# Kernel optimization log

Measured on AMD Instinct MI355X. Metric: run time of the kernel, lower is better.

## Reference

```python
import jax, jax.numpy as jnp
import numpy as np

WINDOW = 128  # window_size from init_kwargs
D = 1024      # input_dim
S = 8192      # seq_len


def setup_inputs() -> dict:
    key = jax.random.key(0)
    k1, k2, k3, k4, k5 = jax.random.split(key, 5)
    bound = 1.0 / np.sqrt(D)
    x = jax.random.normal(k1, (1, S, D), dtype=jnp.float32)
    Wq = jax.random.uniform(k2, (D, D), minval=-bound, maxval=bound, dtype=jnp.float32)
    bq = jax.random.uniform(k3, (D,), minval=-bound, maxval=bound, dtype=jnp.float32)
    Wk = jax.random.uniform(k4, (D, D), minval=-bound, maxval=bound, dtype=jnp.float32)
    bk = jax.random.uniform(k5, (D,), minval=-bound, maxval=bound, dtype=jnp.float32)
    return {"x": x, "Wq": Wq, "bq": bq, "Wk": Wk, "bk": bk}


def reference(x, Wq, bq, Wk, bk):
    # x: [1, S, D]  (original code only works with batch==1)
    xs = x[0]                          # [S, D]
    q = xs @ Wq.T + bq                 # [S, D]
    k = xs @ Wk.T + bk                 # [S, D]
    scores = q @ k.T                   # [S, S] dense, matches original buffer
    t = jnp.arange(S)[:, None]
    s = jnp.arange(S)[None, :]
    # original writes scores only for s in [t-WINDOW, t+WINDOW); elsewhere stays 0
    inwin = (s >= t - WINDOW) & (s < t + WINDOW)
    scores = jnp.where(inwin, scores, 0.0)
    attn = jax.nn.softmax(scores, axis=1)  # softmax INCLUDES the zero entries, as in original
    out = attn @ xs                    # [S, D]
    return out
```

## Files before the change

kernel.cpp:

```cpp
#include <hip/hip_runtime.h>

#define S 8192
#define D 1024
#define WINDOW 128
#define TQ 16
#define UMAX 288
#define BK 32
#define PAD 68
#define BAND 384

typedef __attribute__((ext_vector_type(8))) short short8;
typedef __attribute__((ext_vector_type(4))) float floatx4;
typedef __attribute__((ext_vector_type(4))) unsigned short ushort4v;
typedef unsigned short u16t;

__device__ __forceinline__ float wave_sum(float v) {
  #pragma unroll
  for (int off = 32; off > 0; off >>= 1) v += __shfl_xor(v, off, 64);
  return v;
}
__device__ __forceinline__ float wave_max(float v) {
  #pragma unroll
  for (int off = 32; off > 0; off >>= 1) v = fmaxf(v, __shfl_xor(v, off, 64));
  return v;
}
__device__ __forceinline__ unsigned int f2bf_rn(float f) {
  unsigned int u = __float_as_uint(f);
  return (u + 0x7fffu + ((u >> 16) & 1u)) >> 16;
}

__global__ __launch_bounds__(256) void split_kernel(
    const float* __restrict__ src, u16t* __restrict__ hi, u16t* __restrict__ lo)
{
  int i = (blockIdx.x * 256 + threadIdx.x) * 4;
  float4 v = *(const float4*)(src + i);
  float f[4] = {v.x, v.y, v.z, v.w};
  ushort4v h, l;
  #pragma unroll
  for (int c = 0; c < 4; ++c) {
    unsigned int hb = f2bf_rn(f[c]);
    float hf = __uint_as_float(hb << 16);
    unsigned int lb = f2bf_rn(f[c] - hf);
    h[c] = (u16t)hb;
    l[c] = (u16t)lb;
  }
  *(ushort4v*)(hi + i) = h;
  *(ushort4v*)(lo + i) = l;
}

__global__ __launch_bounds__(256) void transpose_x(const float* __restrict__ x,
                                                   u16t* __restrict__ xT)
{
  __shared__ float tile[64][65];
  const int s0 = blockIdx.x * 64;
  const int d0 = blockIdx.y * 64;
  const int t = threadIdx.x;
  #pragma unroll
  for (int p = 0; p < 4; ++p) {
    int r = (t >> 4) + p * 16;
    int c = (t & 15) * 4;
    float4 v = *(const float4*)(x + (size_t)(s0 + r) * D + d0 + c);
    tile[r][c+0] = v.x; tile[r][c+1] = v.y; tile[r][c+2] = v.z; tile[r][c+3] = v.w;
  }
  __syncthreads();
  #pragma unroll
  for (int p = 0; p < 4; ++p) {
    int dd = (t >> 4) + p * 16;
    int ss = (t & 15) * 4;
    ushort4v o;
    #pragma unroll
    for (int u = 0; u < 4; ++u) o[u] = (u16t)f2bf_rn(tile[ss + u][dd]);
    *(ushort4v*)(xT + (size_t)(d0 + dd) * S + s0 + ss) = o;
  }
}

__global__ __launch_bounds__(256) void gemm_qk(
    const u16t* __restrict__ xhi, const u16t* __restrict__ xlo,
    const u16t* __restrict__ wqhi, const u16t* __restrict__ wqlo,
    const u16t* __restrict__ wkhi, const u16t* __restrict__ wklo,
    const float* __restrict__ bqv, const float* __restrict__ bkv,
    u16t* __restrict__ qh, u16t* __restrict__ ql,
    u16t* __restrict__ kh, u16t* __restrict__ kl)
{
  __shared__ __align__(16) u16t Ah[128 * BK];
  __shared__ __align__(16) u16t Al[128 * BK];
  __shared__ __align__(16) u16t Bh[128 * BK];
  __shared__ __align__(16) u16t Bl[128 * BK];

  const int tid  = threadIdx.x;
  const int lane = tid & 63;
  const int wv   = tid >> 6;
  const int t0   = blockIdx.x * 128;
  const int n0   = blockIdx.y * 128;

  const u16t* whi = blockIdx.z ? wkhi : wqhi;
  const u16t* wlo = blockIdx.z ? wklo : wqlo;
  const float* bias = blockIdx.z ? bkv : bqv;
  u16t* oh = blockIdx.z ? kh : qh;
  u16t* ol = blockIdx.z ? kl : ql;

  floatx4 acc[4][4] = {};

  const int m0w  = (wv & 1) * 64;
  const int n0w  = (wv >> 1) * 64;
  const int srow = lane >> 2;
  const int scol = (((lane & 3) ^ ((lane >> 3) & 3))) * 8;
  const int p8   = (((lane >> 4) ^ ((lane >> 1) & 3))) * 8;

  for (int k0 = 0; k0 < D; k0 += BK) {
    __syncthreads();
    #pragma unroll
    for (int sg = 0; sg < 2; ++sg) {
      int seg  = wv * 2 + sg;
      int arow = t0 + seg * 16 + srow;
      int brow = n0 + seg * 16 + srow;
      size_t ga = (size_t)arow * D + k0 + scol;
      size_t gb = (size_t)brow * D + k0 + scol;
      __builtin_amdgcn_global_load_lds(
          (const __attribute__((address_space(1))) void*)(xhi + ga),
          (__attribute__((address_space(3))) void*)(&Ah[seg * 512]), 16, 0, 0);
      __builtin_amdgcn_global_load_lds(
          (const __attribute__((address_space(1))) void*)(xlo + ga),
          (__attribute__((address_space(3))) void*)(&Al[seg * 512]), 16, 0, 0);
      __builtin_amdgcn_global_load_lds(
          (const __attribute__((address_space(1))) void*)(whi + gb),
          (__attribute__((address_space(3))) void*)(&Bh[seg * 512]), 16, 0, 0);
      __builtin_amdgcn_global_load_lds(
          (const __attribute__((address_space(1))) void*)(wlo + gb),
          (__attribute__((address_space(3))) void*)(&Bl[seg * 512]), 16, 0, 0);
    }
    __syncthreads();

    short8 ah[4], al[4], bh[4], bl[4];
    #pragma unroll
    for (int t = 0; t < 4; ++t) {
      int ar = (m0w + t * 16 + (lane & 15)) * BK + p8;
      int br = (n0w + t * 16 + (lane & 15)) * BK + p8;
      ah[t] = *(const short8*)&Ah[ar];
      al[t] = *(const short8*)&Al[ar];
      bh[t] = *(const short8*)&Bh[br];
      bl[t] = *(const short8*)&Bl[br];
    }
    #pragma unroll
    for (int mt = 0; mt < 4; ++mt)
      #pragma unroll
      for (int nt = 0; nt < 4; ++nt) {
        acc[mt][nt] = __builtin_amdgcn_mfma_f32_16x16x32_bf16(ah[mt], bh[nt], acc[mt][nt], 0, 0, 0);
        acc[mt][nt] = __builtin_amdgcn_mfma_f32_16x16x32_bf16(ah[mt], bl[nt], acc[mt][nt], 0, 0, 0);
        acc[mt][nt] = __builtin_amdgcn_mfma_f32_16x16x32_bf16(al[mt], bh[nt], acc[mt][nt], 0, 0, 0);
      }
  }

  #pragma unroll
  for (int mt = 0; mt < 4; ++mt) {
    #pragma unroll
    for (int nt = 0; nt < 4; ++nt) {
      int n = n0 + n0w + nt * 16 + (lane & 15);
      int m = t0 + m0w + mt * 16 + (lane >> 4) * 4;
      float b = bias[n];
      #pragma unroll
      for (int r = 0; r < 4; ++r) {
        float v = acc[mt][nt][r] + b;
        unsigned int hb = f2bf_rn(v);
        float hf = __uint_as_float(hb << 16);
        unsigned int lb = f2bf_rn(v - hf);
        size_t idx = (size_t)(m + r) * D + n;
        oh[idx] = (u16t)hb;
        ol[idx] = (u16t)lb;
      }
    }
  }
}

__global__ __launch_bounds__(256) void colsum_kernel(const float* __restrict__ x,
                                                     float* __restrict__ xsum)
{
  int d = blockIdx.x * 256 + threadIdx.x;
  int tbase = blockIdx.y * 256;
  float s = 0.f;
  for (int t = 0; t < 256; ++t) s += x[(size_t)(tbase + t) * D + d];
  atomicAdd(&xsum[d], s);
}

__global__ __launch_bounds__(256) void scores_kernel(
    const u16t* __restrict__ qh, const u16t* __restrict__ ql,
    const u16t* __restrict__ kh, const u16t* __restrict__ kl,
    float* __restrict__ band)
{
  __shared__ __align__(16) u16t Ah[128 * BK];
  __shared__ __align__(16) u16t Al[128 * BK];
  __shared__ __align__(16) u16t Bh[128 * BK];
  __shared__ __align__(16) u16t Bl[128 * BK];

  const int tid  = threadIdx.x;
  const int lane = tid & 63;
  const int wv   = tid >> 6;
  const int t0   = blockIdx.x * 128;
  const int jt   = blockIdx.y;
  const int s_base = t0 - 128 + jt * 128;

  floatx4 acc[4][4] = {};

  const int m0w  = (wv & 1) * 64;
  const int n0w  = (wv >> 1) * 64;
  const int srow = lane >> 2;
  const int scol = (((lane & 3) ^ ((lane >> 3) & 3))) * 8;
  const int p8   = (((lane >> 4) ^ ((lane >> 1) & 3))) * 8;

  for (int k0 = 0; k0 < D; k0 += BK) {
    __syncthreads();
    #pragma unroll
    for (int sg = 0; sg < 2; ++sg) {
      int seg  = wv * 2 + sg;
      int arow = t0 + seg * 16 + srow;
      int brow = s_base + seg * 16 + srow;
      brow = min(max(brow, 0), S - 1);
      size_t ga = (size_t)arow * D + k0 + scol;
      size_t gb = (size_t)brow * D + k0 + scol;
      __builtin_amdgcn_global_load_lds(
          (const __attribute__((address_space(1))) void*)(qh + ga),
          (__attribute__((address_space(3))) void*)(&Ah[seg * 512]), 16, 0, 0);
      __builtin_amdgcn_global_load_lds(
          (const __attribute__((address_space(1))) void*)(ql + ga),
          (__attribute__((address_space(3))) void*)(&Al[seg * 512]), 16, 0, 0);
      __builtin_amdgcn_global_load_lds(
          (const __attribute__((address_space(1))) void*)(kh + gb),
          (__attribute__((address_space(3))) void*)(&Bh[seg * 512]), 16, 0, 0);
      __builtin_amdgcn_global_load_lds(
          (const __attribute__((address_space(1))) void*)(kl + gb),
          (__attribute__((address_space(3))) void*)(&Bl[seg * 512]), 16, 0, 0);
    }
    __syncthreads();

    short8 ah[4], al[4], bh[4], bl[4];
    #pragma unroll
    for (int t = 0; t < 4; ++t) {
      int ar = (m0w + t * 16 + (lane & 15)) * BK + p8;
      int br = (n0w + t * 16 + (lane & 15)) * BK + p8;
      ah[t] = *(const short8*)&Ah[ar];
      al[t] = *(const short8*)&Al[ar];
      bh[t] = *(const short8*)&Bh[br];
      bl[t] = *(const short8*)&Bl[br];
    }
    #pragma unroll
    for (int mt = 0; mt < 4; ++mt)
      #pragma unroll
      for (int nt = 0; nt < 4; ++nt) {
        acc[mt][nt] = __builtin_amdgcn_mfma_f32_16x16x32_bf16(ah[mt], bh[nt], acc[mt][nt], 0, 0, 0);
        acc[mt][nt] = __builtin_amdgcn_mfma_f32_16x16x32_bf16(ah[mt], bl[nt], acc[mt][nt], 0, 0, 0);
        acc[mt][nt] = __builtin_amdgcn_mfma_f32_16x16x32_bf16(al[mt], bh[nt], acc[mt][nt], 0, 0, 0);
      }
  }

  #pragma unroll
  for (int mt = 0; mt < 4; ++mt) {
    #pragma unroll
    for (int nt = 0; nt < 4; ++nt) {
      int n_loc = n0w + nt * 16 + (lane & 15);
      int s = s_base + n_loc;
      #pragma unroll
      for (int r = 0; r < 4; ++r) {
        int m_loc = m0w + mt * 16 + (lane >> 4) * 4 + r;
        int t = t0 + m_loc;
        bool inwin = (s >= t - WINDOW) && (s < t + WINDOW) && (s >= 0) && (s < S);
        band[(size_t)t * BAND + jt * 128 + n_loc] = inwin ? acc[mt][nt][r] : 0.f;
      }
    }
  }
}

__global__ __launch_bounds__(256) void softmax_kernel(
    const float* __restrict__ band, u16t* __restrict__ Pb, float* __restrict__ e0d)
{
  const int lane = threadIdx.x & 63;
  const int w    = threadIdx.x >> 6;
  const int t    = blockIdx.x * 4 + w;
  const float* row = band + (size_t)t * BAND;

  float v[6];
  float mx = 0.f;
  #pragma unroll
  for (int i = 0; i < 6; ++i) {
    v[i] = row[i * 64 + lane];
    mx = fmaxf(mx, v[i]);
  }
  mx = wave_max(mx);
  float e0 = __expf(-mx);
  float ss = 0.f;
  #pragma unroll
  for (int i = 0; i < 6; ++i) {
    v[i] = __expf(v[i] - mx);
    ss += v[i];
  }
  ss = wave_sum(ss);
  float dinv = 1.f / (ss + (float)(S - BAND) * e0);
  #pragma unroll
  for (int i = 0; i < 6; ++i)
    Pb[(size_t)t * BAND + i * 64 + lane] = (u16t)f2bf_rn((v[i] - e0) * dinv);
  if (lane == 0) e0d[t] = e0 * dinv;
}

__global__ __launch_bounds__(256) void pv_kernel(
    const u16t* __restrict__ Pb, const u16t* __restrict__ xT,
    const float* __restrict__ e0d, const float* __restrict__ xsum,
    float* __restrict__ out)
{
  __shared__ __align__(16) u16t Ab[128 * BK];
  __shared__ __align__(16) u16t Bb[128 * BK];

  const int tid  = threadIdx.x;
  const int lane = tid & 63;
  const int wv   = tid >> 6;
  const int t0   = blockIdx.x * 128;
  const int d0   = blockIdx.y * 128;
  const int origin = t0 - 128;

  floatx4 acc[4][4] = {};

  const int m0w  = (wv & 1) * 64;
  const int n0w  = (wv >> 1) * 64;
  const int srow = lane >> 2;
  const int scol = (((lane & 3) ^ ((lane >> 3) & 3))) * 8;
  const int p8   = (((lane >> 4) ^ ((lane >> 1) & 3))) * 8;

  for (int k0 = 0; k0 < BAND; k0 += BK) {
    __syncthreads();
    #pragma unroll
    for (int sg = 0; sg < 2; ++sg) {
      int seg  = wv * 2 + sg;
      int arow = t0 + seg * 16 + srow;
      int brow = d0 + seg * 16 + srow;
      int s_g  = origin + k0 + scol;
      s_g = min(max(s_g, 0), S - 8);
      size_t ga = (size_t)arow * BAND + k0 + scol;
      size_t gb = (size_t)brow * S + s_g;
      __builtin_amdgcn_global_load_lds(
          (const __attribute__((address_space(1))) void*)(Pb + ga),
          (__attribute__((address_space(3))) void*)(&Ab[seg * 512]), 16, 0, 0);
      __builtin_amdgcn_global_load_lds(
          (const __attribute__((address_space(1))) void*)(xT + gb),
          (__attribute__((address_space(3))) void*)(&Bb[seg * 512]), 16, 0, 0);
    }
    __syncthreads();

    short8 af[4], bf[4];
    #pragma unroll
    for (int t = 0; t < 4; ++t) {
      int ar = (m0w + t * 16 + (lane & 15)) * BK + p8;
      int br = (n0w + t * 16 + (lane & 15)) * BK + p8;
      af[t] = *(const short8*)&Ab[ar];
      bf[t] = *(const short8*)&Bb[br];
    }
    #pragma unroll
    for (int mt = 0; mt < 4; ++mt)
      #pragma unroll
      for (int nt = 0; nt < 4; ++nt)
        acc[mt][nt] = __builtin_amdgcn_mfma_f32_16x16x32_bf16(af[mt], bf[nt], acc[mt][nt], 0, 0, 0);
  }

  #pragma unroll
  for (int mt = 0; mt < 4; ++mt) {
    #pragma unroll
    for (int nt = 0; nt < 4; ++nt) {
      int n_g = d0 + n0w + nt * 16 + (lane & 15);
      float xs = xsum[n_g];
      #pragma unroll
      for (int r = 0; r < 4; ++r) {
        int m_g = t0 + m0w + mt * 16 + (lane >> 4) * 4 + r;
        out[(size_t)m_g * D + n_g] = acc[mt][nt][r] + e0d[m_g] * xs;
      }
    }
  }
}

__global__ __launch_bounds__(256) void proj_kernel(
    const float* __restrict__ x, const float* __restrict__ Wq,
    const float* __restrict__ bqv, const float* __restrict__ Wk,
    const float* __restrict__ bkv, float* __restrict__ qout,
    float* __restrict__ kout)
{
  __shared__ __align__(16) float xs[BK][PAD];
  __shared__ __align__(16) float wqs[BK][PAD];
  __shared__ __align__(16) float wks[BK][PAD];
  const int tid = threadIdx.x;
  const int tx = tid & 15, ty = tid >> 4;
  const int t0 = blockIdx.x * 64, i0 = blockIdx.y * 64;
  float accq[4][4] = {}, acck[4][4] = {};
  const int lrow0 = tid >> 3, lc4 = (tid & 7) * 4;
  for (int k0 = 0; k0 < D; k0 += BK) {
    __syncthreads();
    #pragma unroll
    for (int p = 0; p < 2; ++p) {
      int row = lrow0 + p * 32;
      float4 a = *(const float4*)(x  + (size_t)(t0 + row) * D + k0 + lc4);
      float4 b = *(const float4*)(Wq + (size_t)(i0 + row) * D + k0 + lc4);
      float4 c = *(const float4*)(Wk + (size_t)(i0 + row) * D + k0 + lc4);
      xs [lc4+0][row]=a.x; xs [lc4+1][row]=a.y; xs [lc4+2][row]=a.z; xs [lc4+3][row]=a.w;
      wqs[lc4+0][row]=b.x; wqs[lc4+1][row]=b.y; wqs[lc4+2][row]=b.z; wqs[lc4+3][row]=b.w;
      wks[lc4+0][row]=c.x; wks[lc4+1][row]=c.y; wks[lc4+2][row]=c.z; wks[lc4+3][row]=c.w;
    }
    __syncthreads();
    #pragma unroll
    for (int kk = 0; kk < BK; ++kk) {
      float4 av = *(const float4*)&xs [kk][ty*4];
      float4 bv = *(const float4*)&wqs[kk][tx*4];
      float4 cv = *(const float4*)&wks[kk][tx*4];
      float a[4] = {av.x, av.y, av.z, av.w};
      float b[4] = {bv.x, bv.y, bv.z, bv.w};
      float c[4] = {cv.x, cv.y, cv.z, cv.w};
      #pragma unroll
      for (int r = 0; r < 4; ++r)
        #pragma unroll
        for (int cc = 0; cc < 4; ++cc) {
          accq[r][cc] = fmaf(a[r], b[cc], accq[r][cc]);
          acck[r][cc] = fmaf(a[r], c[cc], acck[r][cc]);
        }
    }
  }
  float4 bq4 = *(const float4*)(bqv + i0 + tx*4);
  float4 bk4 = *(const float4*)(bkv + i0 + tx*4);
  #pragma unroll
  for (int r = 0; r < 4; ++r) {
    int trow = t0 + ty*4 + r;
    float4 oq = { accq[r][0]+bq4.x, accq[r][1]+bq4.y, accq[r][2]+bq4.z, accq[r][3]+bq4.w };
    float4 ok = { acck[r][0]+bk4.x, acck[r][1]+bk4.y, acck[r][2]+bk4.z, acck[r][3]+bk4.w };
    *(float4*)(qout + (size_t)trow * D + i0 + tx*4) = oq;
    *(float4*)(kout + (size_t)trow * D + i0 + tx*4) = ok;
  }
}

__global__ __launch_bounds__(256) void attn_kernel(
    const float* __restrict__ x, const float* __restrict__ q,
    const float* __restrict__ kmat, const float* __restrict__ xsum,
    float* __restrict__ out)
{
  __shared__ __align__(16) float scl[TQ][UMAX];
  __shared__ float e0s[TQ], dinv[TQ];
  const int tid = threadIdx.x, lane = tid & 63, wv = tid >> 6;
  const int t0 = blockIdx.x * TQ;
  const int lo_u = max(0, t0 - WINDOW);
  const int hi_u = min(S, t0 + TQ - 1 + WINDOW);
  const int ucnt = hi_u - lo_u;
  for (int i = tid; i < TQ * UMAX; i += 256) (&scl[0][0])[i] = 0.f;
  __syncthreads();
  {
    const int tiB = wv * 4;
    float4 qf[4][4];
    #pragma unroll
    for (int g = 0; g < 4; ++g) {
      int t = t0 + tiB + g;
      #pragma unroll
      for (int j = 0; j < 4; ++j)
        qf[g][j] = *(const float4*)(q + (size_t)t * D + lane*4 + j*256);
    }
    const int wlo = max(0, t0 + tiB - WINDOW);
    const int whi = min(S, t0 + tiB + 3 + WINDOW);
    for (int s = wlo; s < whi; ++s) {
      float4 kf[4];
      #pragma unroll
      for (int j = 0; j < 4; ++j)
        kf[j] = *(const float4*)(kmat + (size_t)s * D + lane*4 + j*256);
      float acc[4];
      #pragma unroll
      for (int g = 0; g < 4; ++g) {
        float v = 0.f;
        #pragma unroll
        for (int j = 0; j < 4; ++j) {
          v = fmaf(qf[g][j].x, kf[j].x, v);
          v = fmaf(qf[g][j].y, kf[j].y, v);
          v = fmaf(qf[g][j].z, kf[j].z, v);
          v = fmaf(qf[g][j].w, kf[j].w, v);
        }
        acc[g] = v;
      }
      #pragma unroll
      for (int g = 0; g < 4; ++g) {
        float tot = wave_sum(acc[g]);
        int t = t0 + tiB + g;
        if (lane == 0 && s >= t - WINDOW && s < t + WINDOW)
          scl[tiB + g][s - lo_u] = tot;
      }
    }
  }
  __syncthreads();
  #pragma unroll
  for (int g = 0; g < 4; ++g) {
    int ti = wv * 4 + g;
    int t = t0 + ti;
    int lo = max(0, t - WINDOW), hi = min(S, t + WINDOW);
    int cnt = hi - lo, off = lo - lo_u;
    float m = 0.f;
    for (int i = lane; i < cnt; i += 64) m = fmaxf(m, scl[ti][off + i]);
    m = wave_max(m);
    float e0 = __expf(-m);
    float ssum = 0.f;
    for (int i = lane; i < cnt; i += 64) {
      float e = __expf(scl[ti][off + i] - m);
      ssum += e;
      scl[ti][off + i] = e - e0;
    }
    ssum = wave_sum(ssum);
    if (lane == 0) {
      dinv[ti] = 1.f / (ssum + (float)(S - cnt) * e0);
      e0s[ti] = e0;
    }
  }
  __syncthreads();
  {
    const int c4 = tid * 4;
    float4 acc[TQ];
    #pragma unroll
    for (int ti = 0; ti < TQ; ++ti) acc[ti] = make_float4(0.f, 0.f, 0.f, 0.f);
    for (int su = 0; su < ucnt; su += 4) {
      float4 xr[4];
      #pragma unroll
      for (int u = 0; u < 4; ++u)
        xr[u] = *(const float4*)(x + (size_t)(lo_u + su + u) * D + c4);
      #pragma unroll
      for (int ti = 0; ti < TQ; ++ti) {
        float4 w4 = *(const float4*)&scl[ti][su];
        float wvv[4] = {w4.x, w4.y, w4.z, w4.w};
        #pragma unroll
        for (int u = 0; u < 4; ++u) {
          acc[ti].x = fmaf(wvv[u], xr[u].x, acc[ti].x);
          acc[ti].y = fmaf(wvv[u], xr[u].y, acc[ti].y);
          acc[ti].z = fmaf(wvv[u], xr[u].z, acc[ti].z);
          acc[ti].w = fmaf(wvv[u], xr[u].w, acc[ti].w);
        }
      }
    }
    float4 xsv = *(const float4*)(xsum + c4);
    #pragma unroll
    for (int ti = 0; ti < TQ; ++ti) {
      float e0 = e0s[ti], di = dinv[ti];
      float4 o;
      o.x = (acc[ti].x + e0 * xsv.x) * di;
      o.y = (acc[ti].y + e0 * xsv.y) * di;
      o.z = (acc[ti].z + e0 * xsv.z) * di;
      o.w = (acc[ti].w + e0 * xsv.w) * di;
      *(float4*)(out + (size_t)(t0 + ti) * D + c4) = o;
    }
  }
}

extern "C" void kernel_launch(void* const* d_in, const int* in_sizes, int n_in,
                              void* d_out, int out_size, void* d_ws, size_t ws_size,
                              hipStream_t stream) {
  const float* x  = (const float*)d_in[0];
  const float* Wq = (const float*)d_in[1];
  const float* bq = (const float*)d_in[2];
  const float* Wk = (const float*)d_in[3];
  const float* bk = (const float*)d_in[4];
  float* outp = (float*)d_out;

  const size_t SD = (size_t)S * D;
  const size_t DD = (size_t)D * D;

  float* xsum = (float*)d_ws;
  u16t* xhi = (u16t*)(xsum + D);
  u16t* xlo = xhi + SD;
  u16t* wqh = xlo + SD;
  u16t* wql = wqh + DD;
  u16t* wkh = wql + DD;
  u16t* wkl = wkh + DD;
  u16t* qh  = wkl + DD;
  u16t* ql  = qh + SD;
  u16t* kh  = ql + SD;
  u16t* kl  = kh + SD;
  u16t* xT  = kl + SD;
  size_t needed = (size_t)((char*)(xT + SD) - (char*)d_ws);

  float* band = (float*)xhi;
  u16t*  Pb   = xlo;
  float* e0d  = (float*)(Pb + (size_t)S * BAND);

  hipMemsetAsync(xsum, 0, D * sizeof(float), stream);
  colsum_kernel<<<dim3(D / 256, S / 256), 256, 0, stream>>>(x, xsum);

  if (ws_size >= needed) {
    split_kernel<<<SD / 1024, 256, 0, stream>>>(x,  xhi, xlo);
    split_kernel<<<DD / 1024, 256, 0, stream>>>(Wq, wqh, wql);
    split_kernel<<<DD / 1024, 256, 0, stream>>>(Wk, wkh, wkl);
    transpose_x<<<dim3(S / 64, D / 64), 256, 0, stream>>>(x, xT);
    gemm_qk<<<dim3(S / 128, D / 128, 2), 256, 0, stream>>>(
        xhi, xlo, wqh, wql, wkh, wkl, bq, bk, qh, ql, kh, kl);
    scores_kernel<<<dim3(S / 128, 3), 256, 0, stream>>>(qh, ql, kh, kl, band);
    softmax_kernel<<<S / 4, 256, 0, stream>>>(band, Pb, e0d);
    pv_kernel<<<dim3(S / 128, D / 128), 256, 0, stream>>>(Pb, xT, e0d, xsum, outp);
  } else {
    float* q    = (float*)(xsum + D);
    float* kbuf = q + SD;
    proj_kernel<<<dim3(S / 64, D / 64), 256, 0, stream>>>(x, Wq, bq, Wk, bk, q, kbuf);
    attn_kernel<<<S / TQ, 256, 0, stream>>>(x, q, kbuf, xsum, outp);
  }
}
```

Before: 297.0 us.

## Reassociate scores as x·(WqᵀWk)·xᵀ plus bias terms and fuse prep kernels

Rewrites q·kᵀ as x·M·xᵀ plus rank-one bias terms, with M = Wqᵀ·Wk. This replaces the two S×D×D projection GEMMs with one D×D×D GEMM and a single S×D×D GEMM. The x split, transpose, column sum and the a/b bias dot products are fused into one prep kernel. It also drops the XOR LDS swizzle in all MFMA kernels, which may bring back bank conflicts. Workspace use grows, so a smaller workspace would take the slow fallback path.

```diff
diff --git a/kernel.cpp b/kernel.cpp
--- a/kernel.cpp
+++ b/kernel.cpp
@@ -29,27 +29,32 @@
   return (u + 0x7fffu + ((u >> 16) & 1u)) >> 16;
 }
 
-__global__ __launch_bounds__(256) void split_kernel(
-    const float* __restrict__ src, u16t* __restrict__ hi, u16t* __restrict__ lo)
-{
-  int i = (blockIdx.x * 256 + threadIdx.x) * 4;
-  float4 v = *(const float4*)(src + i);
-  float f[4] = {v.x, v.y, v.z, v.w};
-  ushort4v h, l;
-  #pragma unroll
-  for (int c = 0; c < 4; ++c) {
-    unsigned int hb = f2bf_rn(f[c]);
-    float hf = __uint_as_float(hb << 16);
-    unsigned int lb = f2bf_rn(f[c] - hf);
-    h[c] = (u16t)hb;
-    l[c] = (u16t)lb;
-  }
-  *(ushort4v*)(hi + i) = h;
-  *(ushort4v*)(lo + i) = l;
-}
-
-__global__ __launch_bounds__(256) void transpose_x(const float* __restrict__ x,
-                                                   u16t* __restrict__ xT)
+__global__ __launch_bounds__(256) void uv_kernel(
+    const float* __restrict__ Wq, const float* __restrict__ Wk,
+    const float* __restrict__ bq, const float* __restrict__ bk,
+    float* __restrict__ u, float* __restrict__ v, float* __restrict__ cbuf)
+{
+  const int i = blockIdx.x * 256 + threadIdx.x;
+  const int n0 = blockIdx.y * 128;
+  float us = 0.f, vs = 0.f;
+  for (int n = n0; n < n0 + 128; ++n) {
+    us += Wq[(size_t)n * D + i] * bk[n];
+    vs += Wk[(size_t)n * D + i] * bq[n];
+  }
+  atomicAdd(&u[i], us);
+  atomicAdd(&v[i], vs);
+  if (blockIdx.x == 0 && blockIdx.y == 0) {
+    float cs = 0.f;
+    for (int n = threadIdx.x; n < D; n += 256) cs += bq[n] * bk[n];
+    atomicAdd(cbuf, cs);
+  }
+}
+
+__global__ __launch_bounds__(256) void prep_kernel(
+    const float* __restrict__ x, const float* __restrict__ u,
+    const float* __restrict__ v, u16t* __restrict__ xhi, u16t* __restrict__ xlo,
+    u16t* __restrict__ xT, float* __restrict__ xsum,
+    float* __restrict__ a, float* __restrict__ b)
 {
   __shared__ float tile[64][65];
   const int s0 = blockIdx.x * 64;
@@ -59,8 +64,20 @@
   for (int p = 0; p < 4; ++p) {
     int r = (t >> 4) + p * 16;
     int c = (t & 15) * 4;
-    float4 v = *(const float4*)(x + (size_t)(s0 + r) * D + d0 + c);
-    tile[r][c+0] = v.x; tile[r][c+1] = v.y; tile[r][c+2] = v.z; tile[r][c+3] = v.w;
+    float4 vv = *(const float4*)(x + (size_t)(s0 + r) * D + d0 + c);
+    float f[4] = {vv.x, vv.y, vv.z, vv.w};
+    tile[r][c+0] = vv.x; tile[r][c+1] = vv.y; tile[r][c+2] = vv.z; tile[r][c+3] = vv.w;
+    ushort4v h, l;
+    #pragma unroll
+    for (int e = 0; e < 4; ++e) {
+      unsigned int hb = f2bf_rn(f[e]);
+      float hf = __uint_as_float(hb << 16);
+      h[e] = (u16t)hb;
+      l[e] = (u16t)f2bf_rn(f[e] - hf);
+    }
+    size_t idx = (size_t)(s0 + r) * D + d0 + c;
+    *(ushort4v*)(xhi + idx) = h;
+    *(ushort4v*)(xlo + idx) = l;
   }
   __syncthreads();
   #pragma unroll
@@ -69,18 +86,141 @@
     int ss = (t & 15) * 4;
     ushort4v o;
     #pragma unroll
-    for (int u = 0; u < 4; ++u) o[u] = (u16t)f2bf_rn(tile[ss + u][dd]);
+    for (int e = 0; e < 4; ++e) o[e] = (u16t)f2bf_rn(tile[ss + e][dd]);
     *(ushort4v*)(xT + (size_t)(d0 + dd) * S + s0 + ss) = o;
   }
-}
-
-__global__ __launch_bounds__(256) void gemm_qk(
+  if (t < 64) {
+    float s = 0.f;
+    #pragma unroll 8
+    for (int r = 0; r < 64; ++r) s += tile[r][t];
+    atomicAdd(&xsum[d0 + t], s);
+  } else if (t < 128) {
+    int r = t - 64;
+    float s = 0.f;
+    for (int c = 0; c < 64; ++c) s += tile[r][c] * u[d0 + c];
+    atomicAdd(&a[s0 + r], s);
+  } else if (t < 192) {
+    int r = t - 128;
+    float s = 0.f;
+    for (int c = 0; c < 64; ++c) s += tile[r][c] * v[d0 + c];
+    atomicAdd(&b[s0 + r], s);
+  }
+}
+
+__global__ __launch_bounds__(256) void transposeW_kernel(
+    const float* __restrict__ Wq, const float* __restrict__ Wk,
+    u16t* __restrict__ wqth, u16t* __restrict__ wqtl,
+    u16t* __restrict__ wkth, u16t* __restrict__ wktl)
+{
+  __shared__ float tile[64][65];
+  const float* W = blockIdx.z ? Wk : Wq;
+  u16t* oh = blockIdx.z ? wkth : wqth;
+  u16t* ol = blockIdx.z ? wktl : wqtl;
+  const int n0 = blockIdx.x * 64;
+  const int i0 = blockIdx.y * 64;
+  const int t = threadIdx.x;
+  #pragma unroll
+  for (int p = 0; p < 4; ++p) {
+    int r = (t >> 4) + p * 16;
+    int c = (t & 15) * 4;
+    float4 vv = *(const float4*)(W + (size_t)(n0 + r) * D + i0 + c);
+    tile[r][c+0] = vv.x; tile[r][c+1] = vv.y; tile[r][c+2] = vv.z; tile[r][c+3] = vv.w;
+  }
+  __syncthreads();
+  #pragma unroll
+  for (int p = 0; p < 4; ++p) {
+    int ii = (t >> 4) + p * 16;
+    int nn = (t & 15) * 4;
+    ushort4v h, l;
+    #pragma unroll
+    for (int e = 0; e < 4; ++e) {
+      float f = tile[nn + e][ii];
+      unsigned int hb = f2bf_rn(f);
+      float hf = __uint_as_float(hb << 16);
+      h[e] = (u16t)hb;
+      l[e] = (u16t)f2bf_rn(f - hf);
+    }
+    size_t idx = (size_t)(i0 + ii) * D + n0 + nn;
+    *(ushort4v*)(oh + idx) = h;
+    *(ushort4v*)(ol + idx) = l;
+  }
+}
+
+__global__ __launch_bounds__(256) void m_kernel(
+    const u16t* __restrict__ wqth, const u16t* __restrict__ wqtl,
+    const u16t* __restrict__ wkth, const u16t* __restrict__ wktl,
+    u16t* __restrict__ mh, u16t* __restrict__ ml)
+{
+  __shared__ __align__(16) u16t Mbuf[4][64 * BK];
+
+  const int tid  = threadIdx.x;
+  const int lane = tid & 63;
+  const int wv   = tid >> 6;
+  const int i0   = blockIdx.x * 64;
+  const int j0   = blockIdx.y * 64;
+
+  floatx4 acc[2][2] = {};
+  const int m0w = (wv & 1) * 32;
+  const int n0w = (wv >> 1) * 32;
+  const int srow = lane >> 2;
+  const int scol = (lane & 3) * 8;
+
+  for (int k0 = 0; k0 < D; k0 += BK) {
+    __syncthreads();
+    {
+      const u16t* src = (wv == 0) ? wqth : (wv == 1) ? wqtl : (wv == 2) ? wkth : wktl;
+      const int base  = (wv < 2) ? i0 : j0;
+      #pragma unroll
+      for (int sg = 0; sg < 4; ++sg) {
+        int row = base + sg * 16 + srow;
+        size_t g = (size_t)row * D + k0 + scol;
+        __builtin_amdgcn_global_load_lds(
+            (const __attribute__((address_space(1))) void*)(src + g),
+            (__attribute__((address_space(3))) void*)(&Mbuf[wv][sg * 512]), 16, 0, 0);
+      }
+    }
+    __syncthreads();
+    short8 ah[2], al[2], bh[2], bl[2];
+    #pragma unroll
+    for (int t = 0; t < 2; ++t) {
+      int ar = (m0w + t * 16 + (lane & 15)) * BK + (lane >> 4) * 8;
+      int br = (n0w + t * 16 + (lane & 15)) * BK + (lane >> 4) * 8;
+      ah[t] = *(const short8*)&Mbuf[0][ar];
+      al[t] = *(const short8*)&Mbuf[1][ar];
+      bh[t] = *(const short8*)&Mbuf[2][br];
+      bl[t] = *(const short8*)&Mbuf[3][br];
+    }
+    #pragma unroll
+    for (int mt = 0; mt < 2; ++mt)
+      #pragma unroll
+      for (int nt = 0; nt < 2; ++nt) {
+        acc[mt][nt] = __builtin_amdgcn_mfma_f32_16x16x32_bf16(ah[mt], bh[nt], acc[mt][nt], 0, 0, 0);
+        acc[mt][nt] = __builtin_amdgcn_mfma_f32_16x16x32_bf16(ah[mt], bl[nt], acc[mt][nt], 0, 0, 0);
+        acc[mt][nt] = __builtin_amdgcn_mfma_f32_16x16x32_bf16(al[mt], bh[nt], acc[mt][nt], 0, 0, 0);
+      }
+  }
+  #pragma unroll
+  for (int mt = 0; mt < 2; ++mt)
+    #pragma unroll
+    for (int nt = 0; nt < 2; ++nt) {
+      int j = j0 + n0w + nt * 16 + (lane & 15);
+      int i = i0 + m0w + mt * 16 + (lane >> 4) * 4;
+      #pragma unroll
+      for (int r = 0; r < 4; ++r) {
+        float f = acc[mt][nt][r];
+        unsigned int hb = f2bf_rn(f);
+        float hf = __uint_as_float(hb << 16);
+        size_t idx = (size_t)(i + r) * D + j;
+        mh[idx] = (u16t)hb;
+        ml[idx] = (u16t)f2bf_rn(f - hf);
+      }
+    }
+}
+
+__global__ __launch_bounds__(256) void y_kernel(
     const u16t* __restrict__ xhi, const u16t* __restrict__ xlo,
-    const u16t* __restrict__ wqhi, const u16t* __restrict__ wqlo,
-    const u16t* __restrict__ wkhi, const u16t* __restrict__ wklo,
-    const float* __restrict__ bqv, const float* __restrict__ bkv,
-    u16t* __restrict__ qh, u16t* __restrict__ ql,
-    u16t* __restrict__ kh, u16t* __restrict__ kl)
+    const u16t* __restrict__ mhp, const u16t* __restrict__ mlp,
+    u16t* __restrict__ yh, u16t* __restrict__ yl)
 {
   __shared__ __align__(16) u16t Ah[128 * BK];
   __shared__ __align__(16) u16t Al[128 * BK];
@@ -90,30 +230,22 @@
   const int tid  = threadIdx.x;
   const int lane = tid & 63;
   const int wv   = tid >> 6;
-  const int t0   = blockIdx.x * 128;
-  const int n0   = blockIdx.y * 128;
-
-  const u16t* whi = blockIdx.z ? wkhi : wqhi;
-  const u16t* wlo = blockIdx.z ? wklo : wqlo;
-  const float* bias = blockIdx.z ? bkv : bqv;
-  u16t* oh = blockIdx.z ? kh : qh;
-  u16t* ol = blockIdx.z ? kl : ql;
+  const int s0   = blockIdx.x * 128;
+  const int i0   = blockIdx.y * 128;
 
   floatx4 acc[4][4] = {};
-
   const int m0w  = (wv & 1) * 64;
   const int n0w  = (wv >> 1) * 64;
   const int srow = lane >> 2;
-  const int scol = (((lane & 3) ^ ((lane >> 3) & 3))) * 8;
-  const int p8   = (((lane >> 4) ^ ((lane >> 1) & 3))) * 8;
+  const int scol = (lane & 3) * 8;
 
   for (int k0 = 0; k0 < D; k0 += BK) {
     __syncthreads();
     #pragma unroll
     for (int sg = 0; sg < 2; ++sg) {
       int seg  = wv * 2 + sg;
-      int arow = t0 + seg * 16 + srow;
-      int brow = n0 + seg * 16 + srow;
+      int arow = s0 + seg * 16 + srow;
+      int brow = i0 + seg * 16 + srow;
       size_t ga = (size_t)arow * D + k0 + scol;
       size_t gb = (size_t)brow * D + k0 + scol;
       __builtin_amdgcn_global_load_lds(
@@ -123,19 +255,18 @@
           (const __attribute__((address_space(1))) void*)(xlo + ga),
           (__attribute__((address_space(3))) void*)(&Al[seg * 512]), 16, 0, 0);
       __builtin_amdgcn_global_load_lds(
-          (const __attribute__((address_space(1))) void*)(whi + gb),
+          (const __attribute__((address_space(1))) void*)(mhp + gb),
           (__attribute__((address_space(3))) void*)(&Bh[seg * 512]), 16, 0, 0);
       __builtin_amdgcn_global_load_lds(
-          (const __attribute__((address_space(1))) void*)(wlo + gb),
+          (const __attribute__((address_space(1))) void*)(mlp + gb),
           (__attribute__((address_space(3))) void*)(&Bl[seg * 512]), 16, 0, 0);
     }
     __syncthreads();
-
     short8 ah[4], al[4], bh[4], bl[4];
     #pragma unroll
     for (int t = 0; t < 4; ++t) {
-      int ar = (m0w + t * 16 + (lane & 15)) * BK + p8;
-      int br = (n0w + t * 16 + (lane & 15)) * BK + p8;
+      int ar = (m0w + t * 16 + (lane & 15)) * BK + (lane >> 4) * 8;
+      int br = (n0w + t * 16 + (lane & 15)) * BK + (lane >> 4) * 8;
       ah[t] = *(const short8*)&Ah[ar];
       al[t] = *(const short8*)&Al[ar];
       bh[t] = *(const short8*)&Bh[br];
@@ -150,42 +281,29 @@
         acc[mt][nt] = __builtin_amdgcn_mfma_f32_16x16x32_bf16(al[mt], bh[nt], acc[mt][nt], 0, 0, 0);
       }
   }
-
-  #pragma unroll
-  for (int mt = 0; mt < 4; ++mt) {
+  #pragma unroll
+  for (int mt = 0; mt < 4; ++mt)
     #pragma unroll
     for (int nt = 0; nt < 4; ++nt) {
-      int n = n0 + n0w + nt * 16 + (lane & 15);
-      int m = t0 + m0w + mt * 16 + (lane >> 4) * 4;
-      float b = bias[n];
+      int i = i0 + n0w + nt * 16 + (lane & 15);
+      int s = s0 + m0w + mt * 16 + (lane >> 4) * 4;
       #pragma unroll
       for (int r = 0; r < 4; ++r) {
-        float v = acc[mt][nt][r] + b;
-        unsigned int hb = f2bf_rn(v);
+        float f = acc[mt][nt][r];
+        unsigned int hb = f2bf_rn(f);
         float hf = __uint_as_float(hb << 16);
-        unsigned int lb = f2bf_rn(v - hf);
-        size_t idx = (size_t)(m + r) * D + n;
-        oh[idx] = (u16t)hb;
-        ol[idx] = (u16t)lb;
-      }
-    }
-  }
-}
-
-__global__ __launch_bounds__(256) void colsum_kernel(const float* __restrict__ x,
-                                                     float* __restrict__ xsum)
-{
-  int d = blockIdx.x * 256 + threadIdx.x;
-  int tbase = blockIdx.y * 256;
-  float s = 0.f;
-  for (int t = 0; t < 256; ++t) s += x[(size_t)(tbase + t) * D + d];
-  atomicAdd(&xsum[d], s);
+        size_t idx = (size_t)(s + r) * D + i;
+        yh[idx] = (u16t)hb;
+        yl[idx] = (u16t)f2bf_rn(f - hf);
+      }
+    }
 }
 
 __global__ __launch_bounds__(256) void scores_kernel(
-    const u16t* __restrict__ qh, const u16t* __restrict__ ql,
-    const u16t* __restrict__ kh, const u16t* __restrict__ kl,
-    float* __restrict__ band)
+    const u16t* __restrict__ xhi, const u16t* __restrict__ xlo,
+    const u16t* __restrict__ yh, const u16t* __restrict__ yl,
+    const float* __restrict__ a, const float* __restrict__ b,
+    const float* __restrict__ cbuf, float* __restrict__ band)
 {
   __shared__ __align__(16) u16t Ah[128 * BK];
   __shared__ __align__(16) u16t Al[128 * BK];
@@ -198,14 +316,13 @@
   const int t0   = blockIdx.x * 128;
   const int jt   = blockIdx.y;
   const int s_base = t0 - 128 + jt * 128;
+  const float cval = cbuf[0];
 
   floatx4 acc[4][4] = {};
-
   const int m0w  = (wv & 1) * 64;
   const int n0w  = (wv >> 1) * 64;
   const int srow = lane >> 2;
-  const int scol = (((lane & 3) ^ ((lane >> 3) & 3))) * 8;
-  const int p8   = (((lane >> 4) ^ ((lane >> 1) & 3))) * 8;
+  const int scol = (lane & 3) * 8;
 
   for (int k0 = 0; k0 < D; k0 += BK) {
     __syncthreads();
@@ -218,25 +335,24 @@
       size_t ga = (size_t)arow * D + k0 + scol;
       size_t gb = (size_t)brow * D + k0 + scol;
       __builtin_amdgcn_global_load_lds(
-          (const __attribute__((address_space(1))) void*)(qh + ga),
+          (const __attribute__((address_space(1))) void*)(xhi + ga),
           (__attribute__((address_space(3))) void*)(&Ah[seg * 512]), 16, 0, 0);
       __builtin_amdgcn_global_load_lds(
-          (const __attribute__((address_space(1))) void*)(ql + ga),
+          (const __attribute__((address_space(1))) void*)(xlo + ga),
           (__attribute__((address_space(3))) void*)(&Al[seg * 512]), 16, 0, 0);
       __builtin_amdgcn_global_load_lds(
-          (const __attribute__((address_space(1))) void*)(kh + gb),
+          (const __attribute__((address_space(1))) void*)(yh + gb),
           (__attribute__((address_space(3))) void*)(&Bh[seg * 512]), 16, 0, 0);
       __builtin_amdgcn_global_load_lds(
-          (const __attribute__((address_space(1))) void*)(kl + gb),
+          (const __attribute__((address_space(1))) void*)(yl + gb),
           (__attribute__((address_space(3))) void*)(&Bl[seg * 512]), 16, 0, 0);
     }
     __syncthreads();
-
     short8 ah[4], al[4], bh[4], bl[4];
     #pragma unroll
     for (int t = 0; t < 4; ++t) {
-      int ar = (m0w + t * 16 + (lane & 15)) * BK + p8;
-      int br = (n0w + t * 16 + (lane & 15)) * BK + p8;
+      int ar = (m0w + t * 16 + (lane & 15)) * BK + (lane >> 4) * 8;
+      int br = (n0w + t * 16 + (lane & 15)) * BK + (lane >> 4) * 8;
       ah[t] = *(const short8*)&Ah[ar];
       al[t] = *(const short8*)&Al[ar];
       bh[t] = *(const short8*)&Bh[br];
@@ -251,22 +367,22 @@
         acc[mt][nt] = __builtin_amdgcn_mfma_f32_16x16x32_bf16(al[mt], bh[nt], acc[mt][nt], 0, 0, 0);
       }
   }
-
-  #pragma unroll
-  for (int mt = 0; mt < 4; ++mt) {
+  #pragma unroll
+  for (int mt = 0; mt < 4; ++mt)
     #pragma unroll
     for (int nt = 0; nt < 4; ++nt) {
       int n_loc = n0w + nt * 16 + (lane & 15);
       int s = s_base + n_loc;
+      float bv = (s >= 0 && s < S) ? b[s] : 0.f;
       #pragma unroll
       for (int r = 0; r < 4; ++r) {
         int m_loc = m0w + mt * 16 + (lane >> 4) * 4 + r;
         int t = t0 + m_loc;
         bool inwin = (s >= t - WINDOW) && (s < t + WINDOW) && (s >= 0) && (s < S);
-        band[(size_t)t * BAND + jt * 128 + n_loc] = inwin ? acc[mt][nt][r] : 0.f;
-      }
-    }
-  }
+        float sv = inwin ? (acc[mt][nt][r] + a[t] + bv + cval) : 0.f;
+        band[(size_t)t * BAND + jt * 128 + n_loc] = sv;
+      }
+    }
 }
 
 __global__ __launch_bounds__(256) void softmax_kernel(
@@ -276,7 +392,6 @@
   const int w    = threadIdx.x >> 6;
   const int t    = blockIdx.x * 4 + w;
   const float* row = band + (size_t)t * BAND;
-
   float v[6];
   float mx = 0.f;
   #pragma unroll
@@ -316,12 +431,10 @@
   const int origin = t0 - 128;
 
   floatx4 acc[4][4] = {};
-
   const int m0w  = (wv & 1) * 64;
   const int n0w  = (wv >> 1) * 64;
   const int srow = lane >> 2;
-  const int scol = (((lane & 3) ^ ((lane >> 3) & 3))) * 8;
-  const int p8   = (((lane >> 4) ^ ((lane >> 1) & 3))) * 8;
+  const int scol = (lane & 3) * 8;
 
   for (int k0 = 0; k0 < BAND; k0 += BK) {
     __syncthreads();
@@ -342,12 +455,11 @@
           (__attribute__((address_space(3))) void*)(&Bb[seg * 512]), 16, 0, 0);
     }
     __syncthreads();
-
     short8 af[4], bf[4];
     #pragma unroll
     for (int t = 0; t < 4; ++t) {
-      int ar = (m0w + t * 16 + (lane & 15)) * BK + p8;
-      int br = (n0w + t * 16 + (lane & 15)) * BK + p8;
+      int ar = (m0w + t * 16 + (lane & 15)) * BK + (lane >> 4) * 8;
+      int br = (n0w + t * 16 + (lane & 15)) * BK + (lane >> 4) * 8;
       af[t] = *(const short8*)&Ab[ar];
       bf[t] = *(const short8*)&Bb[br];
     }
@@ -357,9 +469,8 @@
       for (int nt = 0; nt < 4; ++nt)
         acc[mt][nt] = __builtin_amdgcn_mfma_f32_16x16x32_bf16(af[mt], bf[nt], acc[mt][nt], 0, 0, 0);
   }
-
-  #pragma unroll
-  for (int mt = 0; mt < 4; ++mt) {
+  #pragma unroll
+  for (int mt = 0; mt < 4; ++mt)
     #pragma unroll
     for (int nt = 0; nt < 4; ++nt) {
       int n_g = d0 + n0w + nt * 16 + (lane & 15);
@@ -370,7 +481,6 @@
         out[(size_t)m_g * D + n_g] = acc[mt][nt][r] + e0d[m_g] * xs;
       }
     }
-  }
 }
 
 __global__ __launch_bounds__(256) void proj_kernel(
@@ -427,6 +537,16 @@
     *(float4*)(qout + (size_t)trow * D + i0 + tx*4) = oq;
     *(float4*)(kout + (size_t)trow * D + i0 + tx*4) = ok;
   }
+}
+
+__global__ __launch_bounds__(256) void colsum_kernel(const float* __restrict__ x,
+                                                     float* __restrict__ xsum)
+{
+  int d = blockIdx.x * 256 + threadIdx.x;
+  int tbase = blockIdx.y * 256;
+  float s = 0.f;
+  for (int t = 0; t < 256; ++t) s += x[(size_t)(tbase + t) * D + d];
+  atomicAdd(&xsum[d], s);
 }
 
 __global__ __launch_bounds__(256) void attn_kernel(
@@ -557,40 +677,46 @@
   const size_t DD = (size_t)D * D;
 
   float* xsum = (float*)d_ws;
-  u16t* xhi = (u16t*)(xsum + D);
-  u16t* xlo = xhi + SD;
-  u16t* wqh = xlo + SD;
-  u16t* wql = wqh + DD;
-  u16t* wkh = wql + DD;
-  u16t* wkl = wkh + DD;
-  u16t* qh  = wkl + DD;
-  u16t* ql  = qh + SD;
-  u16t* kh  = ql + SD;
-  u16t* kl  = kh + SD;
-  u16t* xT  = kl + SD;
-  size_t needed = (size_t)((char*)(xT + SD) - (char*)d_ws);
-
-  float* band = (float*)xhi;
-  u16t*  Pb   = xlo;
+  float* u    = xsum + D;
+  float* v    = u + D;
+  float* a    = v + D;
+  float* b    = a + S;
+  float* cbuf = b + S;
+  size_t zero_bytes = (size_t)(3 * D + 2 * S + 16) * sizeof(float);
+
+  u16t* xhi  = (u16t*)(cbuf + 16);
+  u16t* xlo  = xhi + SD;
+  u16t* xT   = xlo + SD;
+  u16t* wqth = xT + SD;
+  u16t* wqtl = wqth + DD;
+  u16t* wkth = wqtl + DD;
+  u16t* wktl = wkth + DD;
+  u16t* mh   = wktl + DD;
+  u16t* ml   = mh + DD;
+  u16t* yh   = ml + DD;
+  u16t* yl   = yh + SD;
+  float* band = (float*)(yl + SD);
+  u16t*  Pb   = (u16t*)(band + (size_t)S * BAND);
   float* e0d  = (float*)(Pb + (size_t)S * BAND);
-
-  hipMemsetAsync(xsum, 0, D * sizeof(float), stream);
-  colsum_kernel<<<dim3(D / 256, S / 256), 256, 0, stream>>>(x, xsum);
+  size_t needed = (size_t)((char*)(e0d + S) - (char*)d_ws);
 
   if (ws_size >= needed) {
-    split_kernel<<<SD / 1024, 256, 0, stream>>>(x,  xhi, xlo);
-    split_kernel<<<DD / 1024, 256, 0, stream>>>(Wq, wqh, wql);
-    split_kernel<<<DD / 1024, 256, 0, stream>>>(Wk, wkh, wkl);
-    transpose_x<<<dim3(S / 64, D / 64), 256, 0, stream>>>(x, xT);
-    gemm_qk<<<dim3(S / 128, D / 128, 2), 256, 0, stream>>>(
-        xhi, xlo, wqh, wql, wkh, wkl, bq, bk, qh, ql, kh, kl);
-    scores_kernel<<<dim3(S / 128, 3), 256, 0, stream>>>(qh, ql, kh, kl, band);
+    (void)hipMemsetAsync(d_ws, 0, zero_bytes, stream);
+    uv_kernel<<<dim3(D / 256, 8), 256, 0, stream>>>(Wq, Wk, bq, bk, u, v, cbuf);
+    prep_kernel<<<dim3(S / 64, D / 64), 256, 0, stream>>>(x, u, v, xhi, xlo, xT, xsum, a, b);
+    transposeW_kernel<<<dim3(D / 64, D / 64, 2), 256, 0, stream>>>(Wq, Wk, wqth, wqtl, wkth, wktl);
+    m_kernel<<<dim3(D / 64, D / 64), 256, 0, stream>>>(wqth, wqtl, wkth, wktl, mh, ml);
+    y_kernel<<<dim3(S / 128, D / 128), 256, 0, stream>>>(xhi, xlo, mh, ml, yh, yl);
+    scores_kernel<<<dim3(S / 128, 3), 256, 0, stream>>>(xhi, xlo, yh, yl, a, b, cbuf, band);
     softmax_kernel<<<S / 4, 256, 0, stream>>>(band, Pb, e0d);
     pv_kernel<<<dim3(S / 128, D / 128), 256, 0, stream>>>(Pb, xT, e0d, xsum, outp);
   } else {
-    float* q    = (float*)(xsum + D);
+    float* xs2  = (float*)d_ws;
+    float* q    = xs2 + D;
     float* kbuf = q + SD;
+    (void)hipMemsetAsync(xs2, 0, D * sizeof(float), stream);
+    colsum_kernel<<<dim3(D / 256, S / 256), 256, 0, stream>>>(x, xs2);
     proj_kernel<<<dim3(S / 64, D / 64), 256, 0, stream>>>(x, Wq, bq, Wk, bk, q, kbuf);
-    attn_kernel<<<S / TQ, 256, 0, stream>>>(x, q, kbuf, xsum, outp);
-  }
-}
+    attn_kernel<<<S / TQ, 256, 0, stream>>>(x, q, kbuf, xs2, outp);
+  }
+}
```

After: 269.4 us. -9.3%, faster.
